# Kernel tuning notes

Hardware: AMD Instinct MI355X
Metric: run time of the kernel (lower is better)

Reference implementation:

```python
import jax, jax.numpy as jnp
import numpy as np

N = 50000      # nodes
E = 800000     # edges
D = 128        # input_dim
H = 128        # hidden_dim
C = 10         # num_classes
G = 1024       # graphs in batch
EPS = 1e-5     # BatchNorm eps


def setup_inputs() -> dict:
    key = jax.random.key(0)
    ks = jax.random.split(key, 16)
    p = lambda k, shape: (jax.random.normal(k, shape, dtype=jnp.float32) * 0.05)
    inp = {
        "x": jax.random.normal(ks[0], (N, D), dtype=jnp.float32),
        "edge_index": jax.random.randint(ks[1], (2, E), 0, N, dtype=jnp.int64),
        "batch": jnp.sort(jax.random.randint(ks[2], (N,), 0, G, dtype=jnp.int64)),
        # GraphConv l: out = x @ w_root + segment_sum(x[src])[dst] @ w_rel + b (PyG GraphConv, aggr='add')
        "w_root1": p(ks[3], (D, H)), "w_rel1": p(ks[4], (D, H)), "b1": p(ks[5], (H,)),
        "w_root2": p(ks[6], (H, H)), "w_rel2": p(ks[7], (H, H)), "b2": p(ks[8], (H,)),
        "w_root3": p(ks[9], (H, H)), "w_rel3": p(ks[10], (H, H)), "b3": p(ks[11], (H,)),
        "g1": jnp.ones((H,), jnp.float32), "be1": jnp.zeros((H,), jnp.float32),
        "g2": jnp.ones((H,), jnp.float32), "be2": jnp.zeros((H,), jnp.float32),
        "g3": jnp.ones((H,), jnp.float32), "be3": jnp.zeros((H,), jnp.float32),
        "w_cls": p(ks[12], (H, C)), "b_cls": p(ks[13], (C,)),
    }
    return inp


def _graph_conv(x, src, dst, w_root, w_rel, b):
    # PyG GraphConv: lin_root(x) + lin_rel(sum_{j in N(i)} x_j) + bias
    agg = jax.ops.segment_sum(x[src], dst, num_segments=N)
    return x @ w_root + agg @ w_rel + b


def _batch_norm(x, gamma, beta):
    mean = jnp.mean(x, axis=0)
    var = jnp.var(x, axis=0)
    return (x - mean) * jax.lax.rsqrt(var + EPS) * gamma + beta


def reference(x, edge_index, batch,
              w_root1, w_rel1, b1, w_root2, w_rel2, b2, w_root3, w_rel3, b3,
              g1, be1, g2, be2, g3, be3, w_cls, b_cls):
    src, dst = edge_index[0], edge_index[1]
    h = jax.nn.relu(_batch_norm(_graph_conv(x, src, dst, w_root1, w_rel1, b1), g1, be1))
    h = jax.nn.relu(_batch_norm(_graph_conv(h, src, dst, w_root2, w_rel2, b2), g2, be2))
    h = _batch_norm(_graph_conv(h, src, dst, w_root3, w_rel3, b3), g3, be3)
    # global_mean_pool over graph ids
    sums = jax.ops.segment_sum(h, batch, num_segments=G)
    counts = jax.ops.segment_sum(jnp.ones((N,), h.dtype), batch, num_segments=G)
    pooled = sums / jnp.maximum(counts, 1.0)[:, None]
    # dropout is identity in eval mode
    return pooled @ w_cls + b_cls
```

## Files before the change

### kernel.cpp

```cpp
#include <hip/hip_runtime.h>


constexpr int   NN   = 50000;
constexpr int   NE   = 800000;
constexpr int   DH   = 128;
constexpr int   NC   = 10;
constexpr int   NG   = 1024;
constexpr float EPSV = 1e-5f;
constexpr int   NBUK = (NN + 255) / 256;
constexpr int   BCAP = 5120;
constexpr int   EPB  = 8192;
constexpr int   CSB  = (NE + EPB - 1) / EPB;
constexpr int   NSLOT= 32;

typedef __attribute__((ext_vector_type(8))) short bf16x8;
typedef __attribute__((ext_vector_type(4))) float f32x4;

__device__ __forceinline__ float bflo(unsigned u) { return __uint_as_float(u << 16); }
__device__ __forceinline__ float bfhi(unsigned u) { return __uint_as_float(u & 0xffff0000u); }
__device__ __forceinline__ unsigned short f2bf(float f) {
    unsigned u = __float_as_uint(f);
    return (unsigned short)((u + 0x7fffu + ((u >> 16) & 1u)) >> 16);
}
__device__ __forceinline__ unsigned pk2(float a, float b) {
    return (unsigned)f2bf(a) | ((unsigned)f2bf(b) << 16);
}

__global__ __launch_bounds__(256) void coarse_scatter_kernel(
    const int* __restrict__ src, const int* __restrict__ dst,
    int* __restrict__ bukCnt, int2* __restrict__ pairs)
{
    __shared__ int cnt[NBUK], base[NBUK], cur[NBUK];
    const int tid = threadIdx.x;
    const int e0 = blockIdx.x * EPB;
    const int n  = min(EPB, NE - e0);

    for (int b = tid; b < NBUK; b += 256) cnt[b] = 0;
    __syncthreads();
    for (int i = tid; i < n; i += 256)
        atomicAdd(&cnt[dst[e0 + i] >> 8], 1);
    __syncthreads();
    for (int b = tid; b < NBUK; b += 256) {
        base[b] = (cnt[b] > 0) ? atomicAdd(&bukCnt[b], cnt[b]) : 0;
        cur[b] = 0;
    }
    __syncthreads();
    for (int i = tid; i < n; i += 256) {
        int d = dst[e0 + i], s = src[e0 + i];
        int b = d >> 8;
        int r = atomicAdd(&cur[b], 1);
        int p = base[b] + r;
        if (p >= BCAP) p = BCAP - 1;
        pairs[(size_t)b * BCAP + p] = make_int2(s, d);
    }
}

__global__ __launch_bounds__(256) void bukscan_kernel(
    const int* __restrict__ bukCnt, int* __restrict__ bukBase)
{
    __shared__ int tmp[256];
    int t = threadIdx.x;
    int v = (t < NBUK) ? bukCnt[t] : 0;
    tmp[t] = v;
    __syncthreads();
    for (int off = 1; off < 256; off <<= 1) {
        int u = (t >= off) ? tmp[t - off] : 0;
        __syncthreads();
        tmp[t] += u;
        __syncthreads();
    }
    if (t < NBUK) bukBase[t] = tmp[t] - v;
}

__global__ __launch_bounds__(256) void bucket_finalize_kernel(
    const int2* __restrict__ pairs, const int* __restrict__ bukCnt,
    const int* __restrict__ bukBase, int* __restrict__ offsets,
    int* __restrict__ csr_src)
{
    __shared__ int cnt[256], tmp[256], pos[256];
    const int b = blockIdx.x;
    const int tid = threadIdx.x;
    cnt[tid] = 0;
    __syncthreads();
    const int n = min(bukCnt[b], BCAP);
    const int2* p = pairs + (size_t)b * BCAP;
    for (int i = tid; i < n; i += 256)
        atomicAdd(&cnt[p[i].y & 255], 1);
    __syncthreads();
    int d = cnt[tid];
    tmp[tid] = d;
    __syncthreads();
    for (int off = 1; off < 256; off <<= 1) {
        int u = (tid >= off) ? tmp[tid - off] : 0;
        __syncthreads();
        tmp[tid] += u;
        __syncthreads();
    }
    const int base = bukBase[b];
    int o = base + tmp[tid] - d;
    pos[tid] = o;
    int node = b * 256 + tid;
    if (node < NN) offsets[node] = o;
    if (b == NBUK - 1 && tid == 0) offsets[NN] = NE;
    __syncthreads();
    for (int i = tid; i < n; i += 256) {
        int2 e = p[i];
        int r = atomicAdd(&pos[e.y & 255], 1);
        csr_src[r] = e.x;
    }
}

__global__ __launch_bounds__(256) void convert_x_kernel(
    const float* __restrict__ x, unsigned short* __restrict__ xb)
{
    int i = blockIdx.x * 256 + threadIdx.x;
    if (i >= NN * DH / 8) return;
    const float4* p = reinterpret_cast<const float4*>(x + (size_t)i * 8);
    float4 v0 = p[0], v1 = p[1];
    uint4 o;
    o.x = pk2(v0.x, v0.y); o.y = pk2(v0.z, v0.w);
    o.z = pk2(v1.x, v1.y); o.w = pk2(v1.z, v1.w);
    *reinterpret_cast<uint4*>(xb + (size_t)i * 8) = o;
}

__global__ __launch_bounds__(256) void transpose_w_kernel(
    const float* __restrict__ w0, const float* __restrict__ w1,
    const float* __restrict__ w2, const float* __restrict__ w3,
    const float* __restrict__ w4, const float* __restrict__ w5,
    unsigned short* __restrict__ t0, unsigned short* __restrict__ t1,
    unsigned short* __restrict__ t2, unsigned short* __restrict__ t3,
    unsigned short* __restrict__ t4, unsigned short* __restrict__ t5)
{
    const float* srcs[6] = {w0, w1, w2, w3, w4, w5};
    unsigned short* dsts[6] = {t0, t1, t2, t3, t4, t5};
    int m = blockIdx.x >> 4;
    int sub = blockIdx.x & 15;
    const float* s = srcs[m];
    unsigned short* d = dsts[m];
    for (int it = 0; it < 4; ++it) {
        int i = sub * 1024 + it * 256 + threadIdx.x;
        int c = i & 127, k = i >> 7;
        d[c * 128 + k] = f2bf(s[k * 128 + c]);
    }
}

template <bool TRANSFORM>
__global__ __launch_bounds__(256) void aggregate_kernel(
    const unsigned short* __restrict__ xb, const int* __restrict__ offsets,
    const int* __restrict__ csr_src, const float* __restrict__ sc,
    const float* __restrict__ sh, unsigned short* __restrict__ aggb)
{
    int tid = blockIdx.x * 256 + threadIdx.x;
    int node = tid >> 4;
    if (node >= NN) return;
    int c8 = (tid & 15) * 8;

    float scv[8], shv[8];
    if (TRANSFORM) {
        float4 a = *reinterpret_cast<const float4*>(sc + c8);
        float4 b = *reinterpret_cast<const float4*>(sc + c8 + 4);
        scv[0]=a.x; scv[1]=a.y; scv[2]=a.z; scv[3]=a.w;
        scv[4]=b.x; scv[5]=b.y; scv[6]=b.z; scv[7]=b.w;
        float4 c = *reinterpret_cast<const float4*>(sh + c8);
        float4 d = *reinterpret_cast<const float4*>(sh + c8 + 4);
        shv[0]=c.x; shv[1]=c.y; shv[2]=c.z; shv[3]=c.w;
        shv[4]=d.x; shv[5]=d.y; shv[6]=d.z; shv[7]=d.w;
    }

    float acc[8] = {0.f,0.f,0.f,0.f,0.f,0.f,0.f,0.f};
    auto addv = [&](uint4 v) {
        float f[8] = {bflo(v.x), bfhi(v.x), bflo(v.y), bfhi(v.y),
                      bflo(v.z), bfhi(v.z), bflo(v.w), bfhi(v.w)};
#pragma unroll
        for (int j = 0; j < 8; ++j) {
            float t = TRANSFORM ? fmaxf(fmaf(f[j], scv[j], shv[j]), 0.f) : f[j];
            acc[j] += t;
        }
    };

    int beg = offsets[node], end = offsets[node + 1];
    int e = beg;
    for (; e + 3 < end; e += 4) {
        int s0 = csr_src[e],     s1 = csr_src[e + 1];
        int s2 = csr_src[e + 2], s3 = csr_src[e + 3];
        uint4 v0 = *reinterpret_cast<const uint4*>(xb + (size_t)s0 * DH + c8);
        uint4 v1 = *reinterpret_cast<const uint4*>(xb + (size_t)s1 * DH + c8);
        uint4 v2 = *reinterpret_cast<const uint4*>(xb + (size_t)s2 * DH + c8);
        uint4 v3 = *reinterpret_cast<const uint4*>(xb + (size_t)s3 * DH + c8);
        addv(v0); addv(v1); addv(v2); addv(v3);
    }
    for (; e < end; ++e)
        addv(*reinterpret_cast<const uint4*>(xb + (size_t)csr_src[e] * DH + c8));

    uint4 o;
    o.x = pk2(acc[0], acc[1]); o.y = pk2(acc[2], acc[3]);
    o.z = pk2(acc[4], acc[5]); o.w = pk2(acc[6], acc[7]);
    *reinterpret_cast<uint4*>(aggb + (size_t)node * DH + c8) = o;
}

template <bool TRANSFORM>
__global__ __launch_bounds__(256, 4) void gemm_mfma_kernel(
    const unsigned short* __restrict__ Xb, const unsigned short* __restrict__ Ab,
    const unsigned short* __restrict__ Wrt, const unsigned short* __restrict__ Wlt,
    const float* __restrict__ bias, const float* __restrict__ scIn,
    const float* __restrict__ shIn, unsigned short* __restrict__ OUTb,
    float* __restrict__ stats)
{
    __shared__ unsigned short sW[128][136];
    __shared__ float sScale[DH], sShift[DH];

    const int tid  = threadIdx.x;
    const int lane = tid & 63;
    const int wave = tid >> 6;
    const int row0 = blockIdx.x * 64;
    const int wrow = wave * 16;
    const int l15  = lane & 15;
    const int lk   = (lane >> 4) * 8;

    if (TRANSFORM && tid < DH) {
        sScale[tid] = scIn[tid];
        sShift[tid] = shIn[tid];
    }
#pragma unroll
    for (int i = 0; i < 8; ++i) {
        int f = i * 256 + tid;
        int c = f >> 4;
        int ks = (f & 15) * 8;
        *reinterpret_cast<uint4*>(&sW[c][ks]) =
            *reinterpret_cast<const uint4*>(Wrt + c * 128 + ks);
    }

    f32x4 acc[8];
#pragma unroll
    for (int nt = 0; nt < 8; ++nt) acc[nt] = (f32x4){0.f, 0.f, 0.f, 0.f};

    const int arow = row0 + wrow + l15;
    const bool valid = arow < NN;
    const unsigned short* xptr = Xb + (size_t)arow * DH + lk;
    const unsigned short* aptr = Ab + (size_t)arow * DH + lk;

    uint4 pre[4];
#pragma unroll
    for (int t = 0; t < 4; ++t)
        pre[t] = valid ? *reinterpret_cast<const uint4*>(xptr + t * 32)
                       : make_uint4(0u, 0u, 0u, 0u);

    __syncthreads();

#pragma unroll
    for (int t = 0; t < 4; ++t) {
        uint4 v = pre[t];
        if (TRANSFORM) {
            int cb = t * 32 + lk;
            float f[8] = {bflo(v.x), bfhi(v.x), bflo(v.y), bfhi(v.y),
                          bflo(v.z), bfhi(v.z), bflo(v.w), bfhi(v.w)};
#pragma unroll
            for (int j = 0; j < 8; ++j)
                f[j] = fmaxf(fmaf(f[j], sScale[cb + j], sShift[cb + j]), 0.f);
            v.x = pk2(f[0], f[1]); v.y = pk2(f[2], f[3]);
            v.z = pk2(f[4], f[5]); v.w = pk2(f[6], f[7]);
        }
        bf16x8 a = *reinterpret_cast<bf16x8*>(&v);
        const int kb = t * 32;
#pragma unroll
        for (int nt = 0; nt < 8; ++nt) {
            bf16x8 b = *reinterpret_cast<const bf16x8*>(&sW[nt * 16 + l15][kb + lk]);
            acc[nt] = __builtin_amdgcn_mfma_f32_16x16x32_bf16(a, b, acc[nt], 0, 0, 0);
        }
    }

#pragma unroll
    for (int t = 0; t < 4; ++t)
        pre[t] = valid ? *reinterpret_cast<const uint4*>(aptr + t * 32)
                       : make_uint4(0u, 0u, 0u, 0u);

    __syncthreads();
#pragma unroll
    for (int i = 0; i < 8; ++i) {
        int f = i * 256 + tid;
        int c = f >> 4;
        int ks = (f & 15) * 8;
        *reinterpret_cast<uint4*>(&sW[c][ks]) =
            *reinterpret_cast<const uint4*>(Wlt + c * 128 + ks);
    }
    __syncthreads();

#pragma unroll
    for (int t = 0; t < 4; ++t) {
        uint4 v = pre[t];
        bf16x8 a = *reinterpret_cast<bf16x8*>(&v);
        const int kb = t * 32;
#pragma unroll
        for (int nt = 0; nt < 8; ++nt) {
            bf16x8 b = *reinterpret_cast<const bf16x8*>(&sW[nt * 16 + l15][kb + lk]);
            acc[nt] = __builtin_amdgcn_mfma_f32_16x16x32_bf16(a, b, acc[nt], 0, 0, 0);
        }
    }

    float s_[8] = {0,0,0,0,0,0,0,0}, q_[8] = {0,0,0,0,0,0,0,0};
#pragma unroll
    for (int nt = 0; nt < 8; ++nt) {
        float bvn = bias[nt * 16 + l15];
#pragma unroll
        for (int r = 0; r < 4; ++r) {
            int orow = row0 + wrow + ((lane >> 4) << 2) + r;
            float o = acc[nt][r] + bvn;
            if (orow < NN) {
                OUTb[(size_t)orow * DH + nt * 16 + l15] = f2bf(o);
                s_[nt] += o;
                q_[nt] += o * o;
            }
        }
    }
#pragma unroll
    for (int nt = 0; nt < 8; ++nt) {
        s_[nt] += __shfl_xor(s_[nt], 16, 64);
        s_[nt] += __shfl_xor(s_[nt], 32, 64);
        q_[nt] += __shfl_xor(q_[nt], 16, 64);
        q_[nt] += __shfl_xor(q_[nt], 32, 64);
    }
    __syncthreads();
    float* ldsS = reinterpret_cast<float*>(&sW[0][0]);
    float* ldsQ = ldsS + 512;
    if (lane < 16) {
#pragma unroll
        for (int nt = 0; nt < 8; ++nt) {
            ldsS[wave * DH + nt * 16 + l15] = s_[nt];
            ldsQ[wave * DH + nt * 16 + l15] = q_[nt];
        }
    }
    __syncthreads();
    if (tid < DH) {
        float s = ldsS[tid] + ldsS[DH + tid] + ldsS[2 * DH + tid] + ldsS[3 * DH + tid];
        float q = ldsQ[tid] + ldsQ[DH + tid] + ldsQ[2 * DH + tid] + ldsQ[3 * DH + tid];
        float* slot = stats + (size_t)(blockIdx.x & (NSLOT - 1)) * 256;
        atomicAdd(&slot[tid], s);
        atomicAdd(&slot[128 + tid], q);
    }
}

__global__ __launch_bounds__(128) void finalize_kernel(
    const float* __restrict__ stats, const float* __restrict__ gamma,
    const float* __restrict__ beta, float* __restrict__ sc,
    float* __restrict__ sh)
{
    int j = threadIdx.x;
    float s = 0.f, q = 0.f;
#pragma unroll 8
    for (int sl = 0; sl < NSLOT; ++sl) {
        s += stats[sl * 256 + j];
        q += stats[sl * 256 + 128 + j];
    }
    float mean = s * (1.f / NN);
    float var  = q * (1.f / NN) - mean * mean;
    float sf = rsqrtf(var + EPSV) * gamma[j];
    sc[j] = sf;
    sh[j] = beta[j] - mean * sf;
}

__global__ __launch_bounds__(128) void pool_classify_kernel(
    const unsigned short* __restrict__ Hb, const int* __restrict__ batch,
    const float* __restrict__ sc, const float* __restrict__ sh,
    const float* __restrict__ wcls, const float* __restrict__ bcls,
    float* __restrict__ out)
{
    __shared__ float pl[DH];
    __shared__ int bnd[2];
    int g = blockIdx.x;
    int j = threadIdx.x;
    if (j < 2) {
        int target = g + j;
        int lo = 0, hi = NN;
        while (lo < hi) {
            int mid = (lo + hi) >> 1;
            if (batch[mid] < target) lo = mid + 1; else hi = mid;
        }
        bnd[j] = lo;
    }
    __syncthreads();
    int beg = bnd[0], end = bnd[1];
    float s = 0.f;
    for (int n = beg; n < end; ++n)
        s += bflo((unsigned)Hb[(size_t)n * DH + j]);
    float cnt = (float)(end - beg);
    pl[j] = (s * sc[j] + cnt * sh[j]) / fmaxf(cnt, 1.f);
    __syncthreads();
    if (j < NC) {
        float v = bcls[j];
#pragma unroll 16
        for (int k = 0; k < DH; ++k) v += pl[k] * wcls[k * NC + j];
        out[(size_t)g * NC + j] = v;
    }
}

extern "C" void kernel_launch(void* const* d_in, const int* in_sizes, int n_in,
                              void* d_out, int out_size, void* d_ws, size_t ws_size,
                              hipStream_t stream)
{
    const float* x    = (const float*)d_in[0];
    const int*   ei   = (const int*)d_in[1];
    const int*   batch= (const int*)d_in[2];
    const float* wr1  = (const float*)d_in[3];
    const float* wl1  = (const float*)d_in[4];
    const float* b1   = (const float*)d_in[5];
    const float* wr2  = (const float*)d_in[6];
    const float* wl2  = (const float*)d_in[7];
    const float* b2   = (const float*)d_in[8];
    const float* wr3  = (const float*)d_in[9];
    const float* wl3  = (const float*)d_in[10];
    const float* b3   = (const float*)d_in[11];
    const float* g1   = (const float*)d_in[12];
    const float* be1  = (const float*)d_in[13];
    const float* g2   = (const float*)d_in[14];
    const float* be2  = (const float*)d_in[15];
    const float* g3   = (const float*)d_in[16];
    const float* be3  = (const float*)d_in[17];
    const float* wcls = (const float*)d_in[18];
    const float* bcls = (const float*)d_in[19];
    float* out = (float*)d_out;

    const int* srcp = ei;
    const int* dstp = ei + NE;

    char* ws = (char*)d_ws;
    const size_t featB16 = (size_t)NN * DH * sizeof(unsigned short);
    size_t off = 0;
    auto alloc = [&](size_t bytes) {
        void* p = ws + off;
        off += (bytes + 255) & ~(size_t)255;
        return p;
    };
    unsigned short* xb    = (unsigned short*)alloc(featB16);
    unsigned short* aggb  = (unsigned short*)alloc(featB16);
    unsigned short* hAb   = (unsigned short*)alloc(featB16);
    unsigned short* hBb   = (unsigned short*)alloc(featB16);
    unsigned short* wrt1  = (unsigned short*)alloc(DH * DH * 2);
    unsigned short* wlt1  = (unsigned short*)alloc(DH * DH * 2);
    unsigned short* wrt2  = (unsigned short*)alloc(DH * DH * 2);
    unsigned short* wlt2  = (unsigned short*)alloc(DH * DH * 2);
    unsigned short* wrt3  = (unsigned short*)alloc(DH * DH * 2);
    unsigned short* wlt3  = (unsigned short*)alloc(DH * DH * 2);
    float* statsAll = (float*)alloc(3 * NSLOT * 256 * sizeof(float));
    float* stats1 = statsAll;
    float* stats2 = statsAll + NSLOT * 256;
    float* stats3 = statsAll + 2 * NSLOT * 256;
    int*   offsets = (int*)alloc((NN + 1) * sizeof(int));
    int*   csr_src = (int*)alloc(NE * sizeof(int));
    int2*  pairs   = (int2*)alloc((size_t)NBUK * BCAP * sizeof(int2));
    int*   bukCnt  = (int*)alloc(NBUK * sizeof(int));
    int*   bukBase = (int*)alloc(NBUK * sizeof(int));
    float* sc1 = (float*)alloc(DH * 4); float* sh1 = (float*)alloc(DH * 4);
    float* sc2 = (float*)alloc(DH * 4); float* sh2 = (float*)alloc(DH * 4);
    float* sc3 = (float*)alloc(DH * 4); float* sh3 = (float*)alloc(DH * 4);

    const int aggBlocks  = (NN * 16 + 255) / 256;
    const int gemmBlocks = (NN + 63) / 64;
    const int cvtBlocks  = (NN * DH / 8 + 255) / 256;

    hipMemsetAsync(statsAll, 0, 3 * NSLOT * 256 * sizeof(float), stream);

    hipMemsetAsync(bukCnt, 0, NBUK * sizeof(int), stream);
    coarse_scatter_kernel<<<CSB, 256, 0, stream>>>(srcp, dstp, bukCnt, pairs);
    bukscan_kernel<<<1, 256, 0, stream>>>(bukCnt, bukBase);
    bucket_finalize_kernel<<<NBUK, 256, 0, stream>>>(pairs, bukCnt, bukBase, offsets, csr_src);

    convert_x_kernel<<<cvtBlocks, 256, 0, stream>>>(x, xb);
    transpose_w_kernel<<<96, 256, 0, stream>>>(wr1, wl1, wr2, wl2, wr3, wl3,
                                               wrt1, wlt1, wrt2, wlt2, wrt3, wlt3);

    aggregate_kernel<false><<<aggBlocks, 256, 0, stream>>>(xb, offsets, csr_src, nullptr, nullptr, aggb);
    gemm_mfma_kernel<false><<<gemmBlocks, 256, 0, stream>>>(xb, aggb, wrt1, wlt1, b1, nullptr, nullptr, hAb, stats1);
    finalize_kernel<<<1, 128, 0, stream>>>(stats1, g1, be1, sc1, sh1);

    aggregate_kernel<true><<<aggBlocks, 256, 0, stream>>>(hAb, offsets, csr_src, sc1, sh1, aggb);
    gemm_mfma_kernel<true><<<gemmBlocks, 256, 0, stream>>>(hAb, aggb, wrt2, wlt2, b2, sc1, sh1, hBb, stats2);
    finalize_kernel<<<1, 128, 0, stream>>>(stats2, g2, be2, sc2, sh2);

    aggregate_kernel<true><<<aggBlocks, 256, 0, stream>>>(hBb, offsets, csr_src, sc2, sh2, aggb);
    gemm_mfma_kernel<true><<<gemmBlocks, 256, 0, stream>>>(hBb, aggb, wrt3, wlt3, b3, sc2, sh2, hAb, stats3);
    finalize_kernel<<<1, 128, 0, stream>>>(stats3, g3, be3, sc3, sh3);

    pool_classify_kernel<<<NG, 128, 0, stream>>>(hAb, batch, sc3, sh3, wcls, bcls, out);
}
```

Measured before the change: 225.5 us.

## Fold BN finalize and bucket scan into consumer kernels, unroll gather by 8

Removes the three single-block BN finalize kernels and the single-block bucket scan kernel. Each consumer block (aggregate, gemm, pool) now reduces the 32 stat slots itself, and each bucket_finalize block recomputes the bucket prefix scan. This cuts four serial launches and their tail latency, at the cost of redundant per-block reduction work and global reads. The aggregate gather loop is also unrolled to 8 outstanding row loads to expose more memory parallelism.

```diff
diff --git a/kernel.cpp b/kernel.cpp
--- a/kernel.cpp
+++ b/kernel.cpp
@@ -26,6 +26,23 @@
     return (unsigned)f2bf(a) | ((unsigned)f2bf(b) << 16);
 }
 
+__device__ __forceinline__ void bn_reduce_col(
+    const float* __restrict__ stats, const float* __restrict__ gamma,
+    const float* __restrict__ beta, int j, float& sc, float& sh)
+{
+    float s = 0.f, q = 0.f;
+#pragma unroll 8
+    for (int sl = 0; sl < NSLOT; ++sl) {
+        s += stats[sl * 256 + j];
+        q += stats[sl * 256 + 128 + j];
+    }
+    float mean = s * (1.f / NN);
+    float var  = q * (1.f / NN) - mean * mean;
+    float sf = rsqrtf(var + EPSV) * gamma[j];
+    sc = sf;
+    sh = beta[j] - mean * sf;
+}
+
 __global__ __launch_bounds__(256) void coarse_scatter_kernel(
     const int* __restrict__ src, const int* __restrict__ dst,
     int* __restrict__ bukCnt, int2* __restrict__ pairs)
@@ -55,40 +72,16 @@
     }
 }
 
-__global__ __launch_bounds__(256) void bukscan_kernel(
-    const int* __restrict__ bukCnt, int* __restrict__ bukBase)
-{
-    __shared__ int tmp[256];
-    int t = threadIdx.x;
-    int v = (t < NBUK) ? bukCnt[t] : 0;
-    tmp[t] = v;
-    __syncthreads();
-    for (int off = 1; off < 256; off <<= 1) {
-        int u = (t >= off) ? tmp[t - off] : 0;
-        __syncthreads();
-        tmp[t] += u;
-        __syncthreads();
-    }
-    if (t < NBUK) bukBase[t] = tmp[t] - v;
-}
-
 __global__ __launch_bounds__(256) void bucket_finalize_kernel(
     const int2* __restrict__ pairs, const int* __restrict__ bukCnt,
-    const int* __restrict__ bukBase, int* __restrict__ offsets,
-    int* __restrict__ csr_src)
+    int* __restrict__ offsets, int* __restrict__ csr_src)
 {
     __shared__ int cnt[256], tmp[256], pos[256];
     const int b = blockIdx.x;
     const int tid = threadIdx.x;
-    cnt[tid] = 0;
-    __syncthreads();
-    const int n = min(bukCnt[b], BCAP);
-    const int2* p = pairs + (size_t)b * BCAP;
-    for (int i = tid; i < n; i += 256)
-        atomicAdd(&cnt[p[i].y & 255], 1);
-    __syncthreads();
-    int d = cnt[tid];
-    tmp[tid] = d;
+
+    int bc = (tid < NBUK) ? bukCnt[tid] : 0;
+    tmp[tid] = bc;
     __syncthreads();
     for (int off = 1; off < 256; off <<= 1) {
         int u = (tid >= off) ? tmp[tid - off] : 0;
@@ -96,7 +89,25 @@
         tmp[tid] += u;
         __syncthreads();
     }
-    const int base = bukBase[b];
+    const int base = tmp[b] - bukCnt[b];
+    __syncthreads();
+
+    cnt[tid] = 0;
+    __syncthreads();
+    const int n = min(bukCnt[b], BCAP);
+    const int2* p = pairs + (size_t)b * BCAP;
+    for (int i = tid; i < n; i += 256)
+        atomicAdd(&cnt[p[i].y & 255], 1);
+    __syncthreads();
+    int d = cnt[tid];
+    tmp[tid] = d;
+    __syncthreads();
+    for (int off = 1; off < 256; off <<= 1) {
+        int u = (tid >= off) ? tmp[tid - off] : 0;
+        __syncthreads();
+        tmp[tid] += u;
+        __syncthreads();
+    }
     int o = base + tmp[tid] - d;
     pos[tid] = o;
     int node = b * 256 + tid;
@@ -147,9 +158,17 @@
 template <bool TRANSFORM>
 __global__ __launch_bounds__(256) void aggregate_kernel(
     const unsigned short* __restrict__ xb, const int* __restrict__ offsets,
-    const int* __restrict__ csr_src, const float* __restrict__ sc,
-    const float* __restrict__ sh, unsigned short* __restrict__ aggb)
-{
+    const int* __restrict__ csr_src, const float* __restrict__ statsIn,
+    const float* __restrict__ gamma, const float* __restrict__ beta,
+    unsigned short* __restrict__ aggb)
+{
+    __shared__ float sScale[DH], sShift[DH];
+    if (TRANSFORM) {
+        int j = threadIdx.x;
+        if (j < DH) bn_reduce_col(statsIn, gamma, beta, j, sScale[j], sShift[j]);
+        __syncthreads();
+    }
+
     int tid = blockIdx.x * 256 + threadIdx.x;
     int node = tid >> 4;
     if (node >= NN) return;
@@ -157,14 +176,8 @@
 
     float scv[8], shv[8];
     if (TRANSFORM) {
-        float4 a = *reinterpret_cast<const float4*>(sc + c8);
-        float4 b = *reinterpret_cast<const float4*>(sc + c8 + 4);
-        scv[0]=a.x; scv[1]=a.y; scv[2]=a.z; scv[3]=a.w;
-        scv[4]=b.x; scv[5]=b.y; scv[6]=b.z; scv[7]=b.w;
-        float4 c = *reinterpret_cast<const float4*>(sh + c8);
-        float4 d = *reinterpret_cast<const float4*>(sh + c8 + 4);
-        shv[0]=c.x; shv[1]=c.y; shv[2]=c.z; shv[3]=c.w;
-        shv[4]=d.x; shv[5]=d.y; shv[6]=d.z; shv[7]=d.w;
+#pragma unroll
+        for (int j = 0; j < 8; ++j) { scv[j] = sScale[c8 + j]; shv[j] = sShift[c8 + j]; }
     }
 
     float acc[8] = {0.f,0.f,0.f,0.f,0.f,0.f,0.f,0.f};
@@ -180,14 +193,21 @@
 
     int beg = offsets[node], end = offsets[node + 1];
     int e = beg;
+    for (; e + 7 < end; e += 8) {
+        uint4 v[8];
+#pragma unroll
+        for (int u = 0; u < 8; ++u)
+            v[u] = *reinterpret_cast<const uint4*>(xb + (size_t)csr_src[e + u] * DH + c8);
+#pragma unroll
+        for (int u = 0; u < 8; ++u) addv(v[u]);
+    }
     for (; e + 3 < end; e += 4) {
-        int s0 = csr_src[e],     s1 = csr_src[e + 1];
-        int s2 = csr_src[e + 2], s3 = csr_src[e + 3];
-        uint4 v0 = *reinterpret_cast<const uint4*>(xb + (size_t)s0 * DH + c8);
-        uint4 v1 = *reinterpret_cast<const uint4*>(xb + (size_t)s1 * DH + c8);
-        uint4 v2 = *reinterpret_cast<const uint4*>(xb + (size_t)s2 * DH + c8);
-        uint4 v3 = *reinterpret_cast<const uint4*>(xb + (size_t)s3 * DH + c8);
-        addv(v0); addv(v1); addv(v2); addv(v3);
+        uint4 v[4];
+#pragma unroll
+        for (int u = 0; u < 4; ++u)
+            v[u] = *reinterpret_cast<const uint4*>(xb + (size_t)csr_src[e + u] * DH + c8);
+#pragma unroll
+        for (int u = 0; u < 4; ++u) addv(v[u]);
     }
     for (; e < end; ++e)
         addv(*reinterpret_cast<const uint4*>(xb + (size_t)csr_src[e] * DH + c8));
@@ -202,9 +222,9 @@
 __global__ __launch_bounds__(256, 4) void gemm_mfma_kernel(
     const unsigned short* __restrict__ Xb, const unsigned short* __restrict__ Ab,
     const unsigned short* __restrict__ Wrt, const unsigned short* __restrict__ Wlt,
-    const float* __restrict__ bias, const float* __restrict__ scIn,
-    const float* __restrict__ shIn, unsigned short* __restrict__ OUTb,
-    float* __restrict__ stats)
+    const float* __restrict__ bias, const float* __restrict__ statsIn,
+    const float* __restrict__ gamma, const float* __restrict__ beta,
+    unsigned short* __restrict__ OUTb, float* __restrict__ statsOut)
 {
     __shared__ unsigned short sW[128][136];
     __shared__ float sScale[DH], sShift[DH];
@@ -217,10 +237,9 @@
     const int l15  = lane & 15;
     const int lk   = (lane >> 4) * 8;
 
-    if (TRANSFORM && tid < DH) {
-        sScale[tid] = scIn[tid];
-        sShift[tid] = shIn[tid];
-    }
+    if (TRANSFORM && tid < DH)
+        bn_reduce_col(statsIn, gamma, beta, tid, sScale[tid], sShift[tid]);
+
 #pragma unroll
     for (int i = 0; i < 8; ++i) {
         int f = i * 256 + tid;
@@ -333,41 +352,24 @@
     if (tid < DH) {
         float s = ldsS[tid] + ldsS[DH + tid] + ldsS[2 * DH + tid] + ldsS[3 * DH + tid];
         float q = ldsQ[tid] + ldsQ[DH + tid] + ldsQ[2 * DH + tid] + ldsQ[3 * DH + tid];
-        float* slot = stats + (size_t)(blockIdx.x & (NSLOT - 1)) * 256;
+        float* slot = statsOut + (size_t)(blockIdx.x & (NSLOT - 1)) * 256;
         atomicAdd(&slot[tid], s);
         atomicAdd(&slot[128 + tid], q);
     }
 }
 
-__global__ __launch_bounds__(128) void finalize_kernel(
-    const float* __restrict__ stats, const float* __restrict__ gamma,
-    const float* __restrict__ beta, float* __restrict__ sc,
-    float* __restrict__ sh)
-{
-    int j = threadIdx.x;
-    float s = 0.f, q = 0.f;
-#pragma unroll 8
-    for (int sl = 0; sl < NSLOT; ++sl) {
-        s += stats[sl * 256 + j];
-        q += stats[sl * 256 + 128 + j];
-    }
-    float mean = s * (1.f / NN);
-    float var  = q * (1.f / NN) - mean * mean;
-    float sf = rsqrtf(var + EPSV) * gamma[j];
-    sc[j] = sf;
-    sh[j] = beta[j] - mean * sf;
-}
-
 __global__ __launch_bounds__(128) void pool_classify_kernel(
     const unsigned short* __restrict__ Hb, const int* __restrict__ batch,
-    const float* __restrict__ sc, const float* __restrict__ sh,
-    const float* __restrict__ wcls, const float* __restrict__ bcls,
-    float* __restrict__ out)
+    const float* __restrict__ stats3, const float* __restrict__ gamma,
+    const float* __restrict__ beta, const float* __restrict__ wcls,
+    const float* __restrict__ bcls, float* __restrict__ out)
 {
     __shared__ float pl[DH];
     __shared__ int bnd[2];
     int g = blockIdx.x;
     int j = threadIdx.x;
+    float scj, shj;
+    bn_reduce_col(stats3, gamma, beta, j, scj, shj);
     if (j < 2) {
         int target = g + j;
         int lo = 0, hi = NN;
@@ -383,7 +385,7 @@
     for (int n = beg; n < end; ++n)
         s += bflo((unsigned)Hb[(size_t)n * DH + j]);
     float cnt = (float)(end - beg);
-    pl[j] = (s * sc[j] + cnt * sh[j]) / fmaxf(cnt, 1.f);
+    pl[j] = (s * scj + cnt * shj) / fmaxf(cnt, 1.f);
     __syncthreads();
     if (j < NC) {
         float v = bcls[j];
@@ -448,10 +450,6 @@
     int*   csr_src = (int*)alloc(NE * sizeof(int));
     int2*  pairs   = (int2*)alloc((size_t)NBUK * BCAP * sizeof(int2));
     int*   bukCnt  = (int*)alloc(NBUK * sizeof(int));
-    int*   bukBase = (int*)alloc(NBUK * sizeof(int));
-    float* sc1 = (float*)alloc(DH * 4); float* sh1 = (float*)alloc(DH * 4);
-    float* sc2 = (float*)alloc(DH * 4); float* sh2 = (float*)alloc(DH * 4);
-    float* sc3 = (float*)alloc(DH * 4); float* sh3 = (float*)alloc(DH * 4);
 
     const int aggBlocks  = (NN * 16 + 255) / 256;
     const int gemmBlocks = (NN + 63) / 64;
@@ -461,24 +459,20 @@
 
     hipMemsetAsync(bukCnt, 0, NBUK * sizeof(int), stream);
     coarse_scatter_kernel<<<CSB, 256, 0, stream>>>(srcp, dstp, bukCnt, pairs);
-    bukscan_kernel<<<1, 256, 0, stream>>>(bukCnt, bukBase);
-    bucket_finalize_kernel<<<NBUK, 256, 0, stream>>>(pairs, bukCnt, bukBase, offsets, csr_src);
+    bucket_finalize_kernel<<<NBUK, 256, 0, stream>>>(pairs, bukCnt, offsets, csr_src);
 
     convert_x_kernel<<<cvtBlocks, 256, 0, stream>>>(x, xb);
     transpose_w_kernel<<<96, 256, 0, stream>>>(wr1, wl1, wr2, wl2, wr3, wl3,
                                                wrt1, wlt1, wrt2, wlt2, wrt3, wlt3);
 
-    aggregate_kernel<false><<<aggBlocks, 256, 0, stream>>>(xb, offsets, csr_src, nullptr, nullptr, aggb);
-    gemm_mfma_kernel<false><<<gemmBlocks, 256, 0, stream>>>(xb, aggb, wrt1, wlt1, b1, nullptr, nullptr, hAb, stats1);
-    finalize_kernel<<<1, 128, 0, stream>>>(stats1, g1, be1, sc1, sh1);
-
-    aggregate_kernel<true><<<aggBlocks, 256, 0, stream>>>(hAb, offsets, csr_src, sc1, sh1, aggb);
-    gemm_mfma_kernel<true><<<gemmBlocks, 256, 0, stream>>>(hAb, aggb, wrt2, wlt2, b2, sc1, sh1, hBb, stats2);
-    finalize_kernel<<<1, 128, 0, stream>>>(stats2, g2, be2, sc2, sh2);
-
-    aggregate_kernel<true><<<aggBlocks, 256, 0, stream>>>(hBb, offsets, csr_src, sc2, sh2, aggb);
-    gemm_mfma_kernel<true><<<gemmBlocks, 256, 0, stream>>>(hBb, aggb, wrt3, wlt3, b3, sc2, sh2, hAb, stats3);
-    finalize_kernel<<<1, 128, 0, stream>>>(stats3, g3, be3, sc3, sh3);
-
-    pool_classify_kernel<<<NG, 128, 0, stream>>>(hAb, batch, sc3, sh3, wcls, bcls, out);
-}
+    aggregate_kernel<false><<<aggBlocks, 256, 0, stream>>>(xb, offsets, csr_src, nullptr, nullptr, nullptr, aggb);
+    gemm_mfma_kernel<false><<<gemmBlocks, 256, 0, stream>>>(xb, aggb, wrt1, wlt1, b1, nullptr, nullptr, nullptr, hAb, stats1);
+
+    aggregate_kernel<true><<<aggBlocks, 256, 0, stream>>>(hAb, offsets, csr_src, stats1, g1, be1, aggb);
+    gemm_mfma_kernel<true><<<gemmBlocks, 256, 0, stream>>>(hAb, aggb, wrt2, wlt2, b2, stats1, g1, be1, hBb, stats2);
+
+    aggregate_kernel<true><<<aggBlocks, 256, 0, stream>>>(hBb, offsets, csr_src, stats2, g2, be2, aggb);
+    gemm_mfma_kernel<true><<<gemmBlocks, 256, 0, stream>>>(hBb, aggb, wrt3, wlt3, b3, stats2, g2, be2, hAb, stats3);
+
+    pool_classify_kernel<<<NG, 128, 0, stream>>>(hAb, batch, stats3, g3, be3, wcls, bcls, out);
+}
```

Result: slower. 244.8 us (+8.6%).
